# Kernel optimization log

Measured on AMD Instinct MI355X. Metric: run time of the kernel, lower is better.

Reference implementation:

```python
import jax, jax.numpy as jnp
import numpy as np

EMBED_DIM = 1024
NUM_HEADS = 16
DIM_HEAD = EMBED_DIM // NUM_HEADS


def setup_inputs() -> dict:
    key = jax.random.key(0)
    ks = jax.random.split(key, 9)
    s = 1.0 / np.sqrt(EMBED_DIM)
    x = jax.random.normal(ks[0], (2, 2048, EMBED_DIM), dtype=jnp.float32)
    Wq = jax.random.uniform(ks[1], (EMBED_DIM, EMBED_DIM), jnp.float32, -s, s)
    bq = jax.random.uniform(ks[2], (EMBED_DIM,), jnp.float32, -s, s)
    Wk = jax.random.uniform(ks[3], (EMBED_DIM, EMBED_DIM), jnp.float32, -s, s)
    bk = jax.random.uniform(ks[4], (EMBED_DIM,), jnp.float32, -s, s)
    Wv = jax.random.uniform(ks[5], (EMBED_DIM, EMBED_DIM), jnp.float32, -s, s)
    bv = jax.random.uniform(ks[6], (EMBED_DIM,), jnp.float32, -s, s)
    Wo = jax.random.uniform(ks[7], (EMBED_DIM, EMBED_DIM), jnp.float32, -s, s)
    bo = jax.random.uniform(ks[8], (EMBED_DIM,), jnp.float32, -s, s)
    return {"x": x, "Wq": Wq, "bq": bq, "Wk": Wk, "bk": bk,
            "Wv": Wv, "bv": bv, "Wo": Wo, "bo": bo}


def reference(x, Wq, bq, Wk, bk, Wv, bv, Wo, bo):
    B, S, _ = x.shape
    # Linear layers (torch nn.Linear: x @ W.T + b), reshape to heads
    Q = (x @ Wq.T + bq).reshape(B, S, NUM_HEADS, DIM_HEAD)
    K = (x @ Wk.T + bk).reshape(B, S, NUM_HEADS, DIM_HEAD)
    V = (x @ Wv.T + bv).reshape(B, S, NUM_HEADS, DIM_HEAD)
    scores = jnp.einsum('bqhd,bkhd->bhqk', Q, K) / np.sqrt(DIM_HEAD)
    attn = jax.nn.softmax(scores, axis=-1)
    context = jnp.einsum('bhqk,bkhd->bqhd', attn, V).reshape(B, S, EMBED_DIM)
    return context @ Wo.T + bo
```

## Files before the change

kernel.cpp:

```cpp
#include <hip/hip_runtime.h>
#include <hip/hip_bf16.h>

#define SEQ   2048
#define EMB   1024
#define NHEAD 16
#define DHEAD 64
#define BATCH 2
#define MTOT  (BATCH*SEQ)
#define QT    128
#define KT    64

typedef __attribute__((ext_vector_type(8))) short s8v;
typedef __attribute__((ext_vector_type(4))) short s4v;
typedef __attribute__((ext_vector_type(4))) float f4v;

__device__ __forceinline__ float b2f(short s) {
    union { unsigned u; float f; } v;
    v.u = ((unsigned)(unsigned short)s) << 16;
    return v.f;
}
__device__ __forceinline__ short f2b(float f) {
    union { float fl; unsigned u; } v; v.fl = f;
    unsigned u = v.u;
    u = (u + 0x7fffu + ((u >> 16) & 1u)) >> 16;
    return (short)u;
}
__device__ __forceinline__ unsigned pk2(float a, float b) {
    union { __hip_bfloat162 h; unsigned u; } c;
    c.h = __float22bfloat162_rn(float2{a, b});
    return c.u;
}
__device__ __forceinline__ float b2f_lo(unsigned u) {
    union { unsigned x; float f; } v; v.x = u << 16; return v.f;
}
__device__ __forceinline__ float b2f_hi(unsigned u) {
    union { unsigned x; float f; } v; v.x = u & 0xffff0000u; return v.f;
}

__device__ __forceinline__ void bar_lds() {
    asm volatile("s_waitcnt lgkmcnt(0)\n\ts_barrier" ::: "memory");
}

__device__ __forceinline__ void gl_lds16(const short* g, short* l) {
    __builtin_amdgcn_global_load_lds(
        (const __attribute__((address_space(1))) void*)g,
        (__attribute__((address_space(3))) void*)l, 16, 0, 0);
}

__global__ __launch_bounds__(256)
void cvt_swz(const float* __restrict__ s0, const float* __restrict__ s1,
             const float* __restrict__ s2, const float* __restrict__ s3,
             const float* __restrict__ s4,
             short* __restrict__ d0, short* __restrict__ d1,
             short* __restrict__ d2, short* __restrict__ d3,
             short* __restrict__ d4)
{
    const int seg = blockIdx.y;
    const float* s = seg == 0 ? s0 : seg == 1 ? s1 : seg == 2 ? s2 : seg == 3 ? s3 : s4;
    short*       d = seg == 0 ? d0 : seg == 1 ? d1 : seg == 2 ? d2 : seg == 3 ? d3 : d4;
    const int nchunk = (seg == 0 ? MTOT * EMB : EMB * EMB) / 8;
    const int stride = gridDim.x * 256;
    for (int i = blockIdx.x * 256 + threadIdx.x; i < nchunk; i += stride) {
        const int row = i >> 7;
        const int c   = i & 127;
        const float4 v0 = *(const float4*)(s + (size_t)i * 8);
        const float4 v1 = *(const float4*)(s + (size_t)i * 8 + 4);
        s8v o;
        o[0] = f2b(v0.x); o[1] = f2b(v0.y); o[2] = f2b(v0.z); o[3] = f2b(v0.w);
        o[4] = f2b(v1.x); o[5] = f2b(v1.y); o[6] = f2b(v1.z); o[7] = f2b(v1.w);
        const int cp = (c & ~7) | ((c & 7) ^ (row & 7));
        *(s8v*)(d + (size_t)row * EMB + cp * 8) = o;
    }
}

template<int NT, bool FUSED3>
__global__ __launch_bounds__(256, 3)
void gemm_bb3(const short* __restrict__ A,
              const short* __restrict__ W0, const short* __restrict__ W1, const short* __restrict__ W2,
              const float* __restrict__ B0, const float* __restrict__ B1, const float* __restrict__ B2,
              void* __restrict__ C0, void* __restrict__ C1, void* __restrict__ C2)
{
    constexpr int JN = NT / 32;
    const int K = EMB, N = EMB;
    const int ntiles = EMB / NT;
    const int mat = blockIdx.x / ntiles;
    const int n0  = (blockIdx.x % ntiles) * NT;
    const int m0  = blockIdx.y * 128;
    const short* W  = (mat == 0) ? W0 : (mat == 1 ? W1 : W2);
    const float* Bi = (mat == 0) ? B0 : (mat == 1 ? B1 : B2);
    void*        C  = (mat == 0) ? C0 : (mat == 1 ? C1 : C2);

    __shared__ __align__(16) short As[128 * 64];
    __shared__ __align__(16) short Ws[NT * 64];

    const int tid  = threadIdx.x;
    const int lane = tid & 63;
    const int wave = tid >> 6;
    const int quad = lane >> 4;
    const int l16  = lane & 15;
    const int l8   = l16 & 7;
    const int wm   = wave >> 1;
    const int wn   = wave & 1;

    f4v acc[4][JN] = {};

    const int srow = lane >> 3;
    const int scol = (lane & 7) * 8;

    for (int k0 = 0; k0 < K; k0 += 64) {
        #pragma unroll
        for (int p = 0; p < 4; ++p) {
            const int rbase = wave * 32 + p * 8;
            gl_lds16(A + (size_t)(m0 + rbase + srow) * K + k0 + scol,
                     As + rbase * 64);
        }
        #pragma unroll
        for (int p = 0; p < NT / 32; ++p) {
            const int rbase = wave * (NT / 4) + p * 8;
            gl_lds16(W + (size_t)(n0 + rbase + srow) * K + k0 + scol,
                     Ws + rbase * 64);
        }
        __syncthreads();

        #pragma unroll
        for (int kk = 0; kk < 2; ++kk) {
            const int slot = ((kk * 4 + quad) ^ l8) * 8;
            s8v af[4], wf[JN];
            #pragma unroll
            for (int i = 0; i < 4; ++i)
                af[i] = *(const s8v*)(As + (wm * 64 + i * 16 + l16) * 64 + slot);
            #pragma unroll
            for (int j = 0; j < JN; ++j)
                wf[j] = *(const s8v*)(Ws + (wn * (NT / 2) + j * 16 + l16) * 64 + slot);
            #pragma unroll
            for (int i = 0; i < 4; ++i)
                #pragma unroll
                for (int j = 0; j < JN; ++j)
                    acc[i][j] = __builtin_amdgcn_mfma_f32_16x16x32_bf16(
                        af[i], wf[j], acc[i][j], 0, 0, 0);
        }
        __syncthreads();
    }

    #pragma unroll
    for (int j = 0; j < JN; ++j) {
        const int n = n0 + wn * (NT / 2) + j * 16 + l16;
        const float bv = Bi[n];
        #pragma unroll
        for (int i = 0; i < 4; ++i) {
            const int mb = m0 + wm * 64 + i * 16 + quad * 4;
            if (FUSED3 && mat == 2) {
                const int bb = mb >> 11, s = mb & 2047;
                s4v ov;
                #pragma unroll
                for (int rr = 0; rr < 4; ++rr) ov[rr] = f2b(acc[i][j][rr] + bv);
                *(s4v*)((short*)C + ((size_t)(bb * 1024 + n)) * SEQ + s) = ov;
            } else if (FUSED3) {
                #pragma unroll
                for (int rr = 0; rr < 4; ++rr)
                    ((short*)C)[(size_t)(mb + rr) * N + n] = f2b(acc[i][j][rr] + bv);
            } else {
                #pragma unroll
                for (int rr = 0; rr < 4; ++rr)
                    ((float*)C)[(size_t)(mb + rr) * N + n] = acc[i][j][rr] + bv;
            }
        }
    }
}

__global__ __launch_bounds__(256, 2)
void attn_mfma4(const short* Q, const short* __restrict__ Kg,
                const short* __restrict__ Vt, short* O)
{
    const int blk = blockIdx.x;
    const int qb = blk & 15;
    const int h  = (blk >> 4) & 15;
    const int b  = blk >> 8;
    const int q0 = qb * QT;

    const int tid  = threadIdx.x;
    const int lane = tid & 63;
    const int wave = tid >> 6;
    const int quad = lane >> 4;
    const int l16  = lane & 15;

    __shared__ __align__(16) short Ks[2][64 * 72];
    __shared__ __align__(16) short Vs[2][64 * 72];
    __shared__ __align__(16) short Pt[QT * 72];

    s8v qf[2][2];
    #pragma unroll
    for (int mi = 0; mi < 2; ++mi)
        #pragma unroll
        for (int kk = 0; kk < 2; ++kk)
            qf[mi][kk] = *(const s8v*)(Q + (size_t)(b * SEQ + q0 + wave * 32 + mi * 16 + l16) * EMB
                                         + h * DHEAD + kk * 32 + quad * 8);

    f4v   oacc[4][2] = {};
    float lsum[2] = {};

    const int c = tid & 7, r = tid >> 3;
    const size_t kbase = (size_t)(b * SEQ) * EMB + h * DHEAD;
    const size_t vbase = (size_t)((b * NHEAD + h) * DHEAD) * SEQ;

    s8v ka[2], va[2];
    #pragma unroll
    for (int p = 0; p < 2; ++p) {
        ka[p] = *(const s8v*)(Kg + kbase + (size_t)(r + p * 32) * EMB + c * 8);
        va[p] = *(const s8v*)(Vt + vbase + (size_t)(r + p * 32) * SEQ + c * 8);
    }

    for (int t = 0; t < SEQ / KT; ++t) {
        const int buf = t & 1;
        short* KsB = Ks[buf];
        short* VsB = Vs[buf];

        #pragma unroll
        for (int p = 0; p < 2; ++p) {
            *(s8v*)(KsB + (r + p * 32) * 72 + c * 8) = ka[p];
            *(s8v*)(VsB + (r + p * 32) * 72 + c * 8) = va[p];
        }
        if (t + 1 < SEQ / KT) {
            const int kt2 = (t + 1) * KT;
            #pragma unroll
            for (int p = 0; p < 2; ++p) {
                ka[p] = *(const s8v*)(Kg + kbase + (size_t)(kt2 + r + p * 32) * EMB + c * 8);
                va[p] = *(const s8v*)(Vt + vbase + (size_t)(r + p * 32) * SEQ + kt2 + c * 8);
            }
        }
        bar_lds();

        f4v sc[4][2] = {};
        #pragma unroll
        for (int kk = 0; kk < 2; ++kk) {
            const int ko = kk * 32 + quad * 8;
            s8v kf[4];
            #pragma unroll
            for (int j = 0; j < 4; ++j)
                kf[j] = *(const s8v*)(KsB + (j * 16 + l16) * 72 + ko);
            #pragma unroll
            for (int j = 0; j < 4; ++j)
                #pragma unroll
                for (int mi = 0; mi < 2; ++mi)
                    sc[j][mi] = __builtin_amdgcn_mfma_f32_16x16x32_bf16(
                        kf[j], qf[mi][kk], sc[j][mi], 0, 0, 0);
        }

        #pragma unroll
        for (int j = 0; j < 4; ++j)
            #pragma unroll
            for (int mi = 0; mi < 2; ++mi) {
                const float p0 = __expf(sc[j][mi][0] * 0.125f);
                const float p1 = __expf(sc[j][mi][1] * 0.125f);
                const float p2 = __expf(sc[j][mi][2] * 0.125f);
                const float p3 = __expf(sc[j][mi][3] * 0.125f);
                union { unsigned u[2]; s4v s; } pv;
                pv.u[0] = pk2(p0, p1);
                pv.u[1] = pk2(p2, p3);
                lsum[mi] += (b2f_lo(pv.u[0]) + b2f_hi(pv.u[0]))
                          + (b2f_lo(pv.u[1]) + b2f_hi(pv.u[1]));
                *(s4v*)(Pt + (wave * 32 + mi * 16 + l16) * 72 + j * 16 + quad * 4) = pv.s;
            }

        #pragma unroll
        for (int kk = 0; kk < 2; ++kk) {
            const int ko = kk * 32 + quad * 8;
            s8v pf[2];
            #pragma unroll
            for (int mi = 0; mi < 2; ++mi)
                pf[mi] = *(const s8v*)(Pt + (wave * 32 + mi * 16 + l16) * 72 + ko);
            #pragma unroll
            for (int j = 0; j < 4; ++j) {
                const s8v vf = *(const s8v*)(VsB + (j * 16 + l16) * 72 + ko);
                #pragma unroll
                for (int mi = 0; mi < 2; ++mi)
                    oacc[j][mi] = __builtin_amdgcn_mfma_f32_16x16x32_bf16(
                        vf, pf[mi], oacc[j][mi], 0, 0, 0);
            }
        }
    }

    #pragma unroll
    for (int mi = 0; mi < 2; ++mi) {
        float s = lsum[mi];
        s += __shfl_xor(s, 16);
        s += __shfl_xor(s, 32);
        lsum[mi] = 1.0f / s;
    }

    #pragma unroll
    for (int j = 0; j < 4; ++j)
        #pragma unroll
        for (int mi = 0; mi < 2; ++mi) {
            union { unsigned u[2]; s4v s; } ov;
            ov.u[0] = pk2(oacc[j][mi][0] * lsum[mi], oacc[j][mi][1] * lsum[mi]);
            ov.u[1] = pk2(oacc[j][mi][2] * lsum[mi], oacc[j][mi][3] * lsum[mi]);
            *(s4v*)(Pt + (wave * 32 + mi * 16 + l16) * 72 + j * 16 + quad * 4) = ov.s;
        }

    const int row = tid >> 1;
    const int cb  = (tid & 1) * 4;
    #pragma unroll
    for (int c4 = 0; c4 < 4; ++c4) {
        const int lc = cb + c4;
        const s8v t = *(const s8v*)(Pt + row * 72 + lc * 8);
        *(s8v*)(O + (size_t)(b * SEQ + q0 + row) * EMB + h * DHEAD
                  + ((lc ^ (row & 7)) * 8)) = t;
    }
}

extern "C" void kernel_launch(void* const* d_in, const int* in_sizes, int n_in,
                              void* d_out, int out_size, void* d_ws, size_t ws_size,
                              hipStream_t stream)
{
    const float* x  = (const float*)d_in[0];
    const float* Wq = (const float*)d_in[1];
    const float* bq = (const float*)d_in[2];
    const float* Wk = (const float*)d_in[3];
    const float* bk = (const float*)d_in[4];
    const float* Wv = (const float*)d_in[5];
    const float* bv = (const float*)d_in[6];
    const float* Wo = (const float*)d_in[7];
    const float* bo = (const float*)d_in[8];
    float* out = (float*)d_out;

    short* xb  = (short*)d_ws;
    short* Wqb = xb  + (size_t)MTOT * EMB;
    short* Wkb = Wqb + (size_t)EMB * EMB;
    short* Wvb = Wkb + (size_t)EMB * EMB;
    short* Wob = Wvb + (size_t)EMB * EMB;
    short* Qw  = Wob + (size_t)EMB * EMB;
    short* Kw  = Qw  + (size_t)MTOT * EMB;
    short* Vtw = Kw  + (size_t)MTOT * EMB;

    cvt_swz<<<dim3(512, 5), 256, 0, stream>>>(x, Wq, Wk, Wv, Wo,
                                              xb, Wqb, Wkb, Wvb, Wob);

    gemm_bb3<128, true><<<dim3(24, 32), 256, 0, stream>>>(
        xb, Wqb, Wkb, Wvb, bq, bk, bv, Qw, Kw, Vtw);

    attn_mfma4<<<dim3(BATCH * NHEAD * (SEQ / QT)), 256, 0, stream>>>(Qw, Kw, Vtw, Qw);

    gemm_bb3<64, false><<<dim3(16, 32), 256, 0, stream>>>(
        Qw, Wob, Wob, Wob, bo, bo, bo, out, out, out);
}
```

Before: 198.0 us.

## Fold softmax scale into Q, use exp2, MFMA row sums, XOR-swizzled LDS

Folds the 1/sqrt(d)*log2(e) factor into the Q projection epilogue so attention can use a raw exp2 instead of a scaled __expf. The per-row softmax denominator now comes from an extra MFMA against a ones vector, replacing the scalar bf16 unpack-and-add chain and the cross-lane shuffles. The padded LDS tiles (stride 72) become unpadded stride-64 tiles with XOR swizzling to avoid bank conflicts while cutting LDS use. This adds MFMA work and changes the output address mapping, which now depends on the swizzle being consistent everywhere.

Result: faster. 182.9 us (-7.6%).

```diff
diff --git a/kernel.cpp b/kernel.cpp
--- a/kernel.cpp
+++ b/kernel.cpp
@@ -14,11 +14,6 @@
 typedef __attribute__((ext_vector_type(4))) short s4v;
 typedef __attribute__((ext_vector_type(4))) float f4v;
 
-__device__ __forceinline__ float b2f(short s) {
-    union { unsigned u; float f; } v;
-    v.u = ((unsigned)(unsigned short)s) << 16;
-    return v.f;
-}
 __device__ __forceinline__ short f2b(float f) {
     union { float fl; unsigned u; } v; v.fl = f;
     unsigned u = v.u;
@@ -30,12 +25,12 @@
     c.h = __float22bfloat162_rn(float2{a, b});
     return c.u;
 }
-__device__ __forceinline__ float b2f_lo(unsigned u) {
-    union { unsigned x; float f; } v; v.x = u << 16; return v.f;
-}
-__device__ __forceinline__ float b2f_hi(unsigned u) {
-    union { unsigned x; float f; } v; v.x = u & 0xffff0000u; return v.f;
-}
+
+#if __has_builtin(__builtin_amdgcn_exp2f)
+__device__ __forceinline__ float exp2_fast(float x) { return __builtin_amdgcn_exp2f(x); }
+#else
+__device__ __forceinline__ float exp2_fast(float x) { return exp2f(x); }
+#endif
 
 __device__ __forceinline__ void bar_lds() {
     asm volatile("s_waitcnt lgkmcnt(0)\n\ts_barrier" ::: "memory");
@@ -89,6 +84,7 @@
     const short* W  = (mat == 0) ? W0 : (mat == 1 ? W1 : W2);
     const float* Bi = (mat == 0) ? B0 : (mat == 1 ? B1 : B2);
     void*        C  = (mat == 0) ? C0 : (mat == 1 ? C1 : C2);
+    const float qscale = (FUSED3 && mat == 0) ? 0.18033688f : 1.0f;
 
     __shared__ __align__(16) short As[128 * 64];
     __shared__ __align__(16) short Ws[NT * 64];
@@ -158,7 +154,7 @@
             } else if (FUSED3) {
                 #pragma unroll
                 for (int rr = 0; rr < 4; ++rr)
-                    ((short*)C)[(size_t)(mb + rr) * N + n] = f2b(acc[i][j][rr] + bv);
+                    ((short*)C)[(size_t)(mb + rr) * N + n] = f2b((acc[i][j][rr] + bv) * qscale);
             } else {
                 #pragma unroll
                 for (int rr = 0; rr < 4; ++rr)
@@ -183,10 +179,11 @@
     const int wave = tid >> 6;
     const int quad = lane >> 4;
     const int l16  = lane & 15;
-
-    __shared__ __align__(16) short Ks[2][64 * 72];
-    __shared__ __align__(16) short Vs[2][64 * 72];
-    __shared__ __align__(16) short Pt[QT * 72];
+    const int l8   = l16 & 7;
+
+    __shared__ __align__(16) short Ks[2][64 * 64];
+    __shared__ __align__(16) short Vs[2][64 * 64];
+    __shared__ __align__(16) short Pt[QT * 64];
 
     s8v qf[2][2];
     #pragma unroll
@@ -196,10 +193,14 @@
             qf[mi][kk] = *(const s8v*)(Q + (size_t)(b * SEQ + q0 + wave * 32 + mi * 16 + l16) * EMB
                                          + h * DHEAD + kk * 32 + quad * 8);
 
-    f4v   oacc[4][2] = {};
-    float lsum[2] = {};
+    f4v oacc[4][2] = {};
+    f4v sacc[2]    = {};
+    s8v onef;
+    #pragma unroll
+    for (int i = 0; i < 8; ++i) onef[i] = (short)0x3F80;
 
     const int c = tid & 7, r = tid >> 3;
+    const int swz = (c ^ (r & 7)) * 8;
     const size_t kbase = (size_t)(b * SEQ) * EMB + h * DHEAD;
     const size_t vbase = (size_t)((b * NHEAD + h) * DHEAD) * SEQ;
 
@@ -217,8 +218,8 @@
 
         #pragma unroll
         for (int p = 0; p < 2; ++p) {
-            *(s8v*)(KsB + (r + p * 32) * 72 + c * 8) = ka[p];
-            *(s8v*)(VsB + (r + p * 32) * 72 + c * 8) = va[p];
+            *(s8v*)(KsB + (r + p * 32) * 64 + swz) = ka[p];
+            *(s8v*)(VsB + (r + p * 32) * 64 + swz) = va[p];
         }
         if (t + 1 < SEQ / KT) {
             const int kt2 = (t + 1) * KT;
@@ -233,11 +234,11 @@
         f4v sc[4][2] = {};
         #pragma unroll
         for (int kk = 0; kk < 2; ++kk) {
-            const int ko = kk * 32 + quad * 8;
+            const int ko = ((kk * 4 + quad) ^ l8) * 8;
             s8v kf[4];
             #pragma unroll
             for (int j = 0; j < 4; ++j)
-                kf[j] = *(const s8v*)(KsB + (j * 16 + l16) * 72 + ko);
+                kf[j] = *(const s8v*)(KsB + (j * 16 + l16) * 64 + ko);
             #pragma unroll
             for (int j = 0; j < 4; ++j)
                 #pragma unroll
@@ -250,28 +251,26 @@
         for (int j = 0; j < 4; ++j)
             #pragma unroll
             for (int mi = 0; mi < 2; ++mi) {
-                const float p0 = __expf(sc[j][mi][0] * 0.125f);
-                const float p1 = __expf(sc[j][mi][1] * 0.125f);
-                const float p2 = __expf(sc[j][mi][2] * 0.125f);
-                const float p3 = __expf(sc[j][mi][3] * 0.125f);
                 union { unsigned u[2]; s4v s; } pv;
-                pv.u[0] = pk2(p0, p1);
-                pv.u[1] = pk2(p2, p3);
-                lsum[mi] += (b2f_lo(pv.u[0]) + b2f_hi(pv.u[0]))
-                          + (b2f_lo(pv.u[1]) + b2f_hi(pv.u[1]));
-                *(s4v*)(Pt + (wave * 32 + mi * 16 + l16) * 72 + j * 16 + quad * 4) = pv.s;
+                pv.u[0] = pk2(exp2_fast(sc[j][mi][0]), exp2_fast(sc[j][mi][1]));
+                pv.u[1] = pk2(exp2_fast(sc[j][mi][2]), exp2_fast(sc[j][mi][3]));
+                const int pc = ((j * 2 + (quad >> 1)) ^ l8) * 8 + (quad & 1) * 4;
+                *(s4v*)(Pt + (wave * 32 + mi * 16 + l16) * 64 + pc) = pv.s;
             }
 
         #pragma unroll
         for (int kk = 0; kk < 2; ++kk) {
-            const int ko = kk * 32 + quad * 8;
+            const int ko = ((kk * 4 + quad) ^ l8) * 8;
             s8v pf[2];
             #pragma unroll
-            for (int mi = 0; mi < 2; ++mi)
-                pf[mi] = *(const s8v*)(Pt + (wave * 32 + mi * 16 + l16) * 72 + ko);
+            for (int mi = 0; mi < 2; ++mi) {
+                pf[mi] = *(const s8v*)(Pt + (wave * 32 + mi * 16 + l16) * 64 + ko);
+                sacc[mi] = __builtin_amdgcn_mfma_f32_16x16x32_bf16(
+                    onef, pf[mi], sacc[mi], 0, 0, 0);
+            }
             #pragma unroll
             for (int j = 0; j < 4; ++j) {
-                const s8v vf = *(const s8v*)(VsB + (j * 16 + l16) * 72 + ko);
+                const s8v vf = *(const s8v*)(VsB + (j * 16 + l16) * 64 + ko);
                 #pragma unroll
                 for (int mi = 0; mi < 2; ++mi)
                     oacc[j][mi] = __builtin_amdgcn_mfma_f32_16x16x32_bf16(
@@ -280,32 +279,28 @@
         }
     }
 
-    #pragma unroll
-    for (int mi = 0; mi < 2; ++mi) {
-        float s = lsum[mi];
-        s += __shfl_xor(s, 16);
-        s += __shfl_xor(s, 32);
-        lsum[mi] = 1.0f / s;
-    }
+    float inv[2];
+    #pragma unroll
+    for (int mi = 0; mi < 2; ++mi) inv[mi] = 1.0f / sacc[mi][0];
 
     #pragma unroll
     for (int j = 0; j < 4; ++j)
         #pragma unroll
         for (int mi = 0; mi < 2; ++mi) {
             union { unsigned u[2]; s4v s; } ov;
-            ov.u[0] = pk2(oacc[j][mi][0] * lsum[mi], oacc[j][mi][1] * lsum[mi]);
-            ov.u[1] = pk2(oacc[j][mi][2] * lsum[mi], oacc[j][mi][3] * lsum[mi]);
-            *(s4v*)(Pt + (wave * 32 + mi * 16 + l16) * 72 + j * 16 + quad * 4) = ov.s;
+            ov.u[0] = pk2(oacc[j][mi][0] * inv[mi], oacc[j][mi][1] * inv[mi]);
+            ov.u[1] = pk2(oacc[j][mi][2] * inv[mi], oacc[j][mi][3] * inv[mi]);
+            const int pc = ((j * 2 + (quad >> 1)) ^ l8) * 8 + (quad & 1) * 4;
+            *(s4v*)(Pt + (wave * 32 + mi * 16 + l16) * 64 + pc) = ov.s;
         }
 
     const int row = tid >> 1;
     const int cb  = (tid & 1) * 4;
     #pragma unroll
     for (int c4 = 0; c4 < 4; ++c4) {
-        const int lc = cb + c4;
-        const s8v t = *(const s8v*)(Pt + row * 72 + lc * 8);
-        *(s8v*)(O + (size_t)(b * SEQ + q0 + row) * EMB + h * DHEAD
-                  + ((lc ^ (row & 7)) * 8)) = t;
+        const int pcc = cb + c4;
+        const s8v tt = *(const s8v*)(Pt + row * 64 + pcc * 8);
+        *(s8v*)(O + (size_t)(b * SEQ + q0 + row) * EMB + h * DHEAD + pcc * 8) = tt;
     }
 }
 
```
